# Kernel optimization log

Hardware: AMD Instinct MI355X
Metric: run time of the kernel (lower is better)

Reference implementation:

```python
import jax, jax.numpy as jnp
import numpy as np
import math

N, N0, M, K, CIN, COUT, DIM = 50000, 50000, 32, 15, 64, 64, 3
POINT_INFLUENCE = 0.05
KERNEL_RADIUS = 1.5 * POINT_INFLUENCE  # _INFLUENCE_TO_RADIUS * point_influence


def setup_inputs() -> dict:
    key = jax.random.key(0)
    k1, k2, k3, k4, k5, k6 = jax.random.split(key, 6)
    query_points = jax.random.uniform(k1, (N, DIM), dtype=jnp.float32)
    support_points = jax.random.uniform(k2, (N0, DIM), dtype=jnp.float32)
    # index N0 is the shadow-neighbor index (padding for ragged neighborhoods)
    neighbors = jax.random.randint(k3, (N, M), 0, N0 + 1)
    x = jax.random.normal(k4, (N0, CIN), dtype=jnp.float32)
    # kernel point dispositions inside the kernel ball, center point at origin (fixed='center')
    kp = jax.random.normal(k5, (K, DIM), dtype=jnp.float32)
    kp = kp / jnp.linalg.norm(kp, axis=1, keepdims=True) * (KERNEL_RADIUS * 0.66)
    K_points = kp.at[0].set(0.0)
    # xavier_normal_ init for weight [K, CIN, COUT]
    std = math.sqrt(2.0 / (CIN + COUT))
    weight = jax.random.normal(k6, (K, CIN, COUT), dtype=jnp.float32) * std
    return dict(query_points=query_points, support_points=support_points,
                neighbors=neighbors, x=x, K_points=K_points, weight=weight)


def reference(query_points, support_points, neighbors, x, K_points, weight):
    # shadow point far away + zero shadow feature (handles padded neighbor index N0)
    shadow_pt = jnp.full((1, support_points.shape[1]), 1e6, support_points.dtype)
    sp = jnp.concatenate([support_points, shadow_pt], axis=0)          # [N0+1, 3]
    feats = jnp.concatenate([x, jnp.zeros((1, x.shape[1]), x.dtype)], axis=0)  # [N0+1, CIN]

    # gather & center neighborhoods: [N, M, 3]
    nb_pts = sp[neighbors] - query_points[:, None, :]

    # squared distance to each kernel point without materializing [N,M,K,3]:
    # ||n - k||^2 = ||n||^2 - 2 n.k + ||k||^2  -> [N, M, K]
    sq = (jnp.sum(nb_pts * nb_pts, axis=-1)[:, :, None]
          - 2.0 * jnp.einsum('nmd,kd->nmk', nb_pts, K_points)
          + jnp.sum(K_points * K_points, axis=-1))
    sq = jnp.maximum(sq, 0.0)

    # linear KP influence: clamp(1 - dist / point_influence, min=0) -> transpose to [N, K, M]
    all_weights = jnp.maximum(1.0 - jnp.sqrt(sq) / POINT_INFLUENCE, 0.0)
    all_weights = jnp.swapaxes(all_weights, 1, 2)                      # [N, K, M]

    nb_feats = feats[neighbors]                                        # [N, M, CIN]
    weighted = jnp.matmul(all_weights, nb_feats)                       # [N, K, CIN]
    # sum over kernel points of per-kernel-point matmuls ('sum' aggregation)
    out = jnp.einsum('nkc,kco->no', weighted, weight)                  # [N, COUT]
    return out
```

## Files before the change

kernel.cpp:

```cpp
#include <hip/hip_runtime.h>

#define N_Q   50000
#define N_S   50000
#define M_NB  32
#define K_PTS 15
#define CIN   64
#define COUT  64
#define WPB   4
#define PTS_PER_BLOCK (WPB * 2)

__global__ __launch_bounds__(256) void kpconv_fused2(
    const float* __restrict__ query,
    const float* __restrict__ support,
    const int*   __restrict__ neighbors,
    const float* __restrict__ x,
    const float* __restrict__ kpts,
    const float* __restrict__ weight,
    float*       __restrict__ out)
{
    __shared__ float s_kx[K_PTS], s_ky[K_PTS], s_kz[K_PTS], s_kk[K_PTS];
    __shared__ float s_bc[WPB][CIN];

    const int tid = threadIdx.x;
    if (tid < K_PTS) {
        float kx = kpts[tid * 3 + 0];
        float ky = kpts[tid * 3 + 1];
        float kz = kpts[tid * 3 + 2];
        s_kx[tid] = kx; s_ky[tid] = ky; s_kz[tid] = kz;
        s_kk[tid] = kx * kx + ky * ky + kz * kz;
    }
    __syncthreads();

    const int wv   = tid >> 6;
    const int lane = tid & 63;
    const int base = blockIdx.x * PTS_PER_BLOCK + wv * 2;
    const int h    = lane >> 5;
    const int n    = base + h;
    const int m    = lane & 31;

    const int idx = neighbors[n * M_NB + m];

    float dx = 0.f, dy = 0.f, dz = 0.f, nn = 1e30f;
    if (idx < N_S) {
        dx = support[idx * 3 + 0] - query[n * 3 + 0];
        dy = support[idx * 3 + 1] - query[n * 3 + 1];
        dz = support[idx * 3 + 2] - query[n * 3 + 2];
        nn = dx * dx + dy * dy + dz * dz;
    }

    float toutA = 0.f, toutB = 0.f;

    if (__ballot(nn < 0.0101f)) {
        for (int k = 0; k < K_PTS; ++k) {
            float w = 0.f;
            if (nn < 0.0101f) {
                float dot = dx * s_kx[k] + dy * s_ky[k] + dz * s_kz[k];
                float sq  = fmaxf(nn - 2.f * dot + s_kk[k], 0.f);
                if (sq < 0.0025f)
                    w = 1.f - sqrtf(sq) * 20.f;
            }
            const unsigned long long em = __ballot(w > 0.f);
            if (!em) continue;

            const float* wk = weight + (size_t)k * CIN * COUT;

            unsigned emA = (unsigned)(em & 0xffffffffull);
            if (emA) {
                float racc = 0.f;
                do {
                    const int src = __builtin_ctz(emA); emA &= emA - 1;
                    const float wsrc = __shfl(w,   src);
                    const int   isrc = __shfl(idx, src);
                    racc = fmaf(wsrc, x[(size_t)isrc * CIN + lane], racc);
                } while (emA);
                s_bc[wv][lane] = racc;
                asm volatile("" ::: "memory");
                float p0 = 0.f, p1 = 0.f, p2 = 0.f, p3 = 0.f;
                #pragma unroll 8
                for (int c = 0; c < CIN; c += 4) {
                    p0 = fmaf(s_bc[wv][c + 0], wk[(c + 0) * COUT + lane], p0);
                    p1 = fmaf(s_bc[wv][c + 1], wk[(c + 1) * COUT + lane], p1);
                    p2 = fmaf(s_bc[wv][c + 2], wk[(c + 2) * COUT + lane], p2);
                    p3 = fmaf(s_bc[wv][c + 3], wk[(c + 3) * COUT + lane], p3);
                }
                toutA += (p0 + p1) + (p2 + p3);
                asm volatile("" ::: "memory");
            }

            unsigned emB = (unsigned)(em >> 32);
            if (emB) {
                float racc = 0.f;
                do {
                    const int src = 32 + __builtin_ctz(emB); emB &= emB - 1;
                    const float wsrc = __shfl(w,   src);
                    const int   isrc = __shfl(idx, src);
                    racc = fmaf(wsrc, x[(size_t)isrc * CIN + lane], racc);
                } while (emB);
                s_bc[wv][lane] = racc;
                asm volatile("" ::: "memory");
                float p0 = 0.f, p1 = 0.f, p2 = 0.f, p3 = 0.f;
                #pragma unroll 8
                for (int c = 0; c < CIN; c += 4) {
                    p0 = fmaf(s_bc[wv][c + 0], wk[(c + 0) * COUT + lane], p0);
                    p1 = fmaf(s_bc[wv][c + 1], wk[(c + 1) * COUT + lane], p1);
                    p2 = fmaf(s_bc[wv][c + 2], wk[(c + 2) * COUT + lane], p2);
                    p3 = fmaf(s_bc[wv][c + 3], wk[(c + 3) * COUT + lane], p3);
                }
                toutB += (p0 + p1) + (p2 + p3);
                asm volatile("" ::: "memory");
            }
        }
    }

    out[(size_t)(base + 0) * COUT + lane] = toutA;
    out[(size_t)(base + 1) * COUT + lane] = toutB;
}

extern "C" void kernel_launch(void* const* d_in, const int* in_sizes, int n_in,
                              void* d_out, int out_size, void* d_ws, size_t ws_size,
                              hipStream_t stream) {
    const float* query     = (const float*)d_in[0];
    const float* support   = (const float*)d_in[1];
    const int*   neighbors = (const int*)  d_in[2];
    const float* x         = (const float*)d_in[3];
    const float* kpts      = (const float*)d_in[4];
    const float* weight    = (const float*)d_in[5];
    float*       out       = (float*)d_out;

    kpconv_fused2<<<N_Q / PTS_PER_BLOCK, 256, 0, stream>>>(
        query, support, neighbors, x, kpts, weight, out);
}
```

Measured before the change: 30.03 us.

## Vectorize weight matvec with float4 loads and cross-lane reduction, shrink blocks

Each lane now computes four output channels for a quarter of the input channels, loading weight rows as float4 and combining partial sums with xor shuffles across lane groups, instead of one output channel over all 64 inputs. This cuts the number of weight load instructions and LDS broadcast reads per matvec. Block size drops from 4 to 2 waves, with more blocks launched, and outputs are written as float4 by 32 lanes. It adds shuffle reductions per active kernel point.

```diff
diff --git a/kernel.cpp b/kernel.cpp
--- a/kernel.cpp
+++ b/kernel.cpp
@@ -6,10 +6,9 @@
 #define K_PTS 15
 #define CIN   64
 #define COUT  64
-#define WPB   4
-#define PTS_PER_BLOCK (WPB * 2)
+#define WPB   2
 
-__global__ __launch_bounds__(256) void kpconv_fused2(
+__global__ __launch_bounds__(128) void kpconv_fused4(
     const float* __restrict__ query,
     const float* __restrict__ support,
     const int*   __restrict__ neighbors,
@@ -33,7 +32,7 @@
 
     const int wv   = tid >> 6;
     const int lane = tid & 63;
-    const int base = blockIdx.x * PTS_PER_BLOCK + wv * 2;
+    const int base = blockIdx.x * (WPB * 2) + wv * 2;
     const int h    = lane >> 5;
     const int n    = base + h;
     const int m    = lane & 31;
@@ -48,7 +47,11 @@
         nn = dx * dx + dy * dy + dz * dz;
     }
 
-    float toutA = 0.f, toutB = 0.f;
+    const int og = (lane & 15) * 4;
+    const int cg = lane >> 4;
+
+    float4 toutA = make_float4(0.f, 0.f, 0.f, 0.f);
+    float4 toutB = make_float4(0.f, 0.f, 0.f, 0.f);
 
     if (__ballot(nn < 0.0101f)) {
         for (int k = 0; k < K_PTS; ++k) {
@@ -63,6 +66,7 @@
             if (!em) continue;
 
             const float* wk = weight + (size_t)k * CIN * COUT;
+            const float* wq = wk + cg * COUT + og;
 
             unsigned emA = (unsigned)(em & 0xffffffffull);
             if (emA) {
@@ -75,15 +79,26 @@
                 } while (emA);
                 s_bc[wv][lane] = racc;
                 asm volatile("" ::: "memory");
-                float p0 = 0.f, p1 = 0.f, p2 = 0.f, p3 = 0.f;
-                #pragma unroll 8
-                for (int c = 0; c < CIN; c += 4) {
-                    p0 = fmaf(s_bc[wv][c + 0], wk[(c + 0) * COUT + lane], p0);
-                    p1 = fmaf(s_bc[wv][c + 1], wk[(c + 1) * COUT + lane], p1);
-                    p2 = fmaf(s_bc[wv][c + 2], wk[(c + 2) * COUT + lane], p2);
-                    p3 = fmaf(s_bc[wv][c + 3], wk[(c + 3) * COUT + lane], p3);
+                float4 a0 = make_float4(0.f,0.f,0.f,0.f);
+                float4 a1 = make_float4(0.f,0.f,0.f,0.f);
+                #pragma unroll
+                for (int i = 0; i < 16; i += 2) {
+                    const float4 v0 = *(const float4*)(wq + (i + 0) * 4 * COUT);
+                    const float4 v1 = *(const float4*)(wq + (i + 1) * 4 * COUT);
+                    const float xc0 = s_bc[wv][cg + 4 * i];
+                    const float xc1 = s_bc[wv][cg + 4 * i + 4];
+                    a0.x = fmaf(xc0, v0.x, a0.x); a0.y = fmaf(xc0, v0.y, a0.y);
+                    a0.z = fmaf(xc0, v0.z, a0.z); a0.w = fmaf(xc0, v0.w, a0.w);
+                    a1.x = fmaf(xc1, v1.x, a1.x); a1.y = fmaf(xc1, v1.y, a1.y);
+                    a1.z = fmaf(xc1, v1.z, a1.z); a1.w = fmaf(xc1, v1.w, a1.w);
                 }
-                toutA += (p0 + p1) + (p2 + p3);
+                a0.x += a1.x; a0.y += a1.y; a0.z += a1.z; a0.w += a1.w;
+                a0.x += __shfl_xor(a0.x, 16); a0.y += __shfl_xor(a0.y, 16);
+                a0.z += __shfl_xor(a0.z, 16); a0.w += __shfl_xor(a0.w, 16);
+                a0.x += __shfl_xor(a0.x, 32); a0.y += __shfl_xor(a0.y, 32);
+                a0.z += __shfl_xor(a0.z, 32); a0.w += __shfl_xor(a0.w, 32);
+                toutA.x += a0.x; toutA.y += a0.y;
+                toutA.z += a0.z; toutA.w += a0.w;
                 asm volatile("" ::: "memory");
             }
 
@@ -98,22 +113,35 @@
                 } while (emB);
                 s_bc[wv][lane] = racc;
                 asm volatile("" ::: "memory");
-                float p0 = 0.f, p1 = 0.f, p2 = 0.f, p3 = 0.f;
-                #pragma unroll 8
-                for (int c = 0; c < CIN; c += 4) {
-                    p0 = fmaf(s_bc[wv][c + 0], wk[(c + 0) * COUT + lane], p0);
-                    p1 = fmaf(s_bc[wv][c + 1], wk[(c + 1) * COUT + lane], p1);
-                    p2 = fmaf(s_bc[wv][c + 2], wk[(c + 2) * COUT + lane], p2);
-                    p3 = fmaf(s_bc[wv][c + 3], wk[(c + 3) * COUT + lane], p3);
+                float4 a0 = make_float4(0.f,0.f,0.f,0.f);
+                float4 a1 = make_float4(0.f,0.f,0.f,0.f);
+                #pragma unroll
+                for (int i = 0; i < 16; i += 2) {
+                    const float4 v0 = *(const float4*)(wq + (i + 0) * 4 * COUT);
+                    const float4 v1 = *(const float4*)(wq + (i + 1) * 4 * COUT);
+                    const float xc0 = s_bc[wv][cg + 4 * i];
+                    const float xc1 = s_bc[wv][cg + 4 * i + 4];
+                    a0.x = fmaf(xc0, v0.x, a0.x); a0.y = fmaf(xc0, v0.y, a0.y);
+                    a0.z = fmaf(xc0, v0.z, a0.z); a0.w = fmaf(xc0, v0.w, a0.w);
+                    a1.x = fmaf(xc1, v1.x, a1.x); a1.y = fmaf(xc1, v1.y, a1.y);
+                    a1.z = fmaf(xc1, v1.z, a1.z); a1.w = fmaf(xc1, v1.w, a1.w);
                 }
-                toutB += (p0 + p1) + (p2 + p3);
+                a0.x += a1.x; a0.y += a1.y; a0.z += a1.z; a0.w += a1.w;
+                a0.x += __shfl_xor(a0.x, 16); a0.y += __shfl_xor(a0.y, 16);
+                a0.z += __shfl_xor(a0.z, 16); a0.w += __shfl_xor(a0.w, 16);
+                a0.x += __shfl_xor(a0.x, 32); a0.y += __shfl_xor(a0.y, 32);
+                a0.z += __shfl_xor(a0.z, 32); a0.w += __shfl_xor(a0.w, 32);
+                toutB.x += a0.x; toutB.y += a0.y;
+                toutB.z += a0.z; toutB.w += a0.w;
                 asm volatile("" ::: "memory");
             }
         }
     }
 
-    out[(size_t)(base + 0) * COUT + lane] = toutA;
-    out[(size_t)(base + 1) * COUT + lane] = toutB;
+    float4* rowA = (float4*)(out + (size_t)(base + 0) * COUT);
+    float4* rowB = (float4*)(out + (size_t)(base + 1) * COUT);
+    if (lane < 16)       rowA[lane]      = toutA;
+    else if (lane < 32)  rowB[lane - 16] = toutB;
 }
 
 extern "C" void kernel_launch(void* const* d_in, const int* in_sizes, int n_in,
@@ -127,6 +155,6 @@
     const float* weight    = (const float*)d_in[5];
     float*       out       = (float*)d_out;
 
-    kpconv_fused2<<<N_Q / PTS_PER_BLOCK, 256, 0, stream>>>(
+    kpconv_fused4<<<N_Q / 4, 128, 0, stream>>>(
         query, support, neighbors, x, kpts, weight, out);
 }
```

Measured after the change: 27.87 us. 7.2% less time.
